# Kernel tuning notes

Hardware: AMD Instinct MI355X
Metric: run time of the kernel (lower is better)

## Reference

```python
import jax, jax.numpy as jnp
import numpy as np

B, L, DM, H, PD = 2, 1024, 512, 8, 64
D = DM // H  # head_dim = 64
NEG = -10000.0


def setup_inputs() -> dict:
    key = jax.random.key(0)
    ks = jax.random.split(key, 12)
    s = 1.0 / np.sqrt(DM)
    sp = 1.0 / np.sqrt(PD)
    return {
        "x": jax.random.normal(ks[0], (B, L, DM), dtype=jnp.float32),
        "z": jax.random.normal(ks[1], (B, L, L, PD), dtype=jnp.float32),
        "residue_mask": jnp.ones((B, L), dtype=bool),
        "Wq": jax.random.normal(ks[2], (DM, DM), dtype=jnp.float32) * s,
        "bq": jnp.zeros((DM,), dtype=jnp.float32),
        "Wk": jax.random.normal(ks[3], (DM, DM), dtype=jnp.float32) * s,
        "bk": jnp.zeros((DM,), dtype=jnp.float32),
        "Wv": jax.random.normal(ks[4], (DM, DM), dtype=jnp.float32) * s,
        "bv": jnp.zeros((DM,), dtype=jnp.float32),
        "Wo": jax.random.normal(ks[5], (DM, DM), dtype=jnp.float32) * s,
        "bo": jnp.zeros((DM,), dtype=jnp.float32),
        "Wpb": jax.random.normal(ks[6], (PD, H), dtype=jnp.float32) * sp,
    }


def reference(x, z, residue_mask, Wq, bq, Wk, bk, Wv, bv, Wo, bo, Wpb):
    b, l, c = x.shape
    scale = 1.0 / np.sqrt(D)
    # projections -> (B, H, L, D)
    q = (x @ Wq + bq).reshape(b, l, H, D).transpose(0, 2, 1, 3)
    k = (x @ Wk + bk).reshape(b, l, H, D).transpose(0, 2, 1, 3)
    v = (x @ Wv + bv).reshape(b, l, H, D).transpose(0, 2, 1, 3)
    # pair bias: (B, L, L, PD) @ (PD, H) -> (B, H, L, L)
    bias = jnp.einsum('bijp,ph->bhij', z, Wpb)
    logits = jnp.einsum('bhid,bhjd->bhij', q, k) * scale + bias
    key_ok = residue_mask[:, None, None, :]
    query_ok = residue_mask[:, None, :, None]
    logits = jnp.where(key_ok, logits, NEG)
    logits = jnp.where(query_ok, logits, NEG)
    attn = jax.nn.softmax(logits, axis=-1)
    out = jnp.einsum('bhij,bhjd->bhid', attn, v)
    out = out.transpose(0, 2, 1, 3).reshape(b, l, c)
    return out @ Wo + bo
```

## Files before the change

### kernel.cpp

```cpp
#include <hip/hip_runtime.h>

typedef __bf16 bf16;
typedef __attribute__((ext_vector_type(4))) __bf16 bf16x4;
typedef __attribute__((ext_vector_type(8))) __bf16 bf16x8;
typedef __attribute__((ext_vector_type(4))) float f32x4;
typedef __attribute__((ext_vector_type(4))) _Float16 f16x4;
typedef __attribute__((ext_vector_type(2))) _Float16 f16x2;

#define B_   2
#define L_   1024
#define DM_  512
#define H_   8
#define D_   64
#define PD_  64
#define NEG_VAL -10000.0f

#define WTPB_N (16*64)

static __device__ __forceinline__ f32x4 mfma_bf16(bf16x8 a, bf16x8 b, f32x4 c) {
  return __builtin_amdgcn_mfma_f32_16x16x32_bf16(a, b, c, 0, 0, 0);
}

__global__ __launch_bounds__(256) void prep_kernel(
    const float* __restrict__ x, const float* __restrict__ Wq, const float* __restrict__ Wk,
    const float* __restrict__ Wv, const float* __restrict__ Wo, const float* __restrict__ Wpb,
    bf16* __restrict__ xb, bf16* __restrict__ Wt, bf16* __restrict__ Wto, bf16* __restrict__ Wtpb) {
  __shared__ float td[32][33];
  int bid = blockIdx.x, tid = threadIdx.x;
  if (bid < 1024) {
    int r = tid >> 3, c4 = (tid & 7) * 4;
    const float* src;
    bf16* dstbase;
    int n0, k0, srcol;
    if (bid < 768) {
      int nt2 = bid >> 4, kt = bid & 15;
      n0 = nt2 * 32; k0 = kt * 32;
      int sel = n0 >> 9;
      src = sel == 0 ? Wq : (sel == 1 ? Wk : Wv);
      srcol = n0 & 511;
      dstbase = Wt + (long)n0 * 512;
    } else {
      int t2 = bid - 768;
      int nt2 = t2 >> 4, kt = t2 & 15;
      n0 = nt2 * 32; k0 = kt * 32;
      src = Wo; srcol = n0;
      dstbase = Wto + (long)n0 * 512;
    }
    f32x4 v = *reinterpret_cast<const f32x4*>(src + (long)(k0 + r) * 512 + srcol + c4);
#pragma unroll
    for (int e = 0; e < 4; ++e) td[r][c4 + e] = v[e];
    __syncthreads();
    int nl = tid >> 3, k4 = (tid & 7) * 4;
    bf16x4 o;
#pragma unroll
    for (int e = 0; e < 4; ++e) o[e] = (bf16)td[k4 + e][nl];
    *reinterpret_cast<bf16x4*>(dstbase + (long)nl * 512 + k0 + k4) = o;
  } else if (bid < 2048) {
    int base = (bid - 1024) * 1024 + tid * 4;
    f32x4 v = *reinterpret_cast<const f32x4*>(x + base);
    bf16x4 o;
#pragma unroll
    for (int e = 0; e < 4; ++e) o[e] = (bf16)v[e];
    *reinterpret_cast<bf16x4*>(xb + base) = o;
  } else {
    for (int t = tid; t < WTPB_N; t += 256) {
      int n = t >> 6, kk = t & 63;
      Wtpb[t] = (n < 8) ? (bf16)Wpb[kk * 8 + n] : (bf16)0.0f;
    }
  }
}

__global__ __launch_bounds__(256) void qkv_gemm(
    const bf16* __restrict__ xb, const bf16* __restrict__ Wt,
    const float* __restrict__ bq, const float* __restrict__ bk, const float* __restrict__ bv,
    bf16* __restrict__ qb, bf16* __restrict__ kb, bf16* __restrict__ vT) {
  int wid = blockIdx.x * 4 + (threadIdx.x >> 6);
  int lane = threadIdx.x & 63;
  int mt = wid / 48, nt = wid - mt * 48;
  int row0 = mt * 32, col0 = nt * 32;
  int lr = lane & 15, lg = lane >> 4;
  const bf16* a0p = xb + (row0 + lr) * 512 + lg * 8;
  const bf16* a1p = a0p + 16 * 512;
  const bf16* b0p = Wt + (col0 + lr) * 512 + lg * 8;
  const bf16* b1p = b0p + 16 * 512;
  f32x4 acc00 = {0.f,0.f,0.f,0.f}, acc01 = acc00, acc10 = acc00, acc11 = acc00;
#pragma unroll
  for (int kk = 0; kk < 512; kk += 32) {
    bf16x8 a0 = *reinterpret_cast<const bf16x8*>(a0p + kk);
    bf16x8 a1 = *reinterpret_cast<const bf16x8*>(a1p + kk);
    bf16x8 b0 = *reinterpret_cast<const bf16x8*>(b0p + kk);
    bf16x8 b1 = *reinterpret_cast<const bf16x8*>(b1p + kk);
    acc00 = mfma_bf16(a0, b0, acc00);
    acc01 = mfma_bf16(a0, b1, acc01);
    acc10 = mfma_bf16(a1, b0, acc10);
    acc11 = mfma_bf16(a1, b1, acc11);
  }
#pragma unroll
  for (int ni = 0; ni < 2; ++ni) {
    int col = col0 + ni * 16 + lr;
    int wsel = col >> 9;
    int ncol = col & 511;
    int h = ncol >> 6, d = ncol & 63;
    const float* bias = wsel == 0 ? bq : (wsel == 1 ? bk : bv);
    float bval = bias[ncol];
#pragma unroll
    for (int mi = 0; mi < 2; ++mi) {
      f32x4 acc = (mi == 0) ? (ni == 0 ? acc00 : acc01) : (ni == 0 ? acc10 : acc11);
      int m0 = row0 + mi * 16 + lg * 4;
      int bidx = m0 >> 10, l0 = m0 & 1023;
      if (wsel == 2) {
        bf16x4 pv;
#pragma unroll
        for (int r = 0; r < 4; ++r) pv[r] = (bf16)(acc[r] + bval);
        *reinterpret_cast<bf16x4*>(vT + ((long)(bidx * H_ + h) * D_ + d) * L_ + l0) = pv;
      } else if (wsel == 0) {
#pragma unroll
        for (int r = 0; r < 4; ++r)
          qb[((long)(bidx * H_ + h) * L_ + l0 + r) * D_ + d] = (bf16)((acc[r] + bval) * 0.125f);
      } else {
#pragma unroll
        for (int r = 0; r < 4; ++r)
          kb[((long)(bidx * H_ + h) * L_ + l0 + r) * D_ + d] = (bf16)(acc[r] + bval);
      }
    }
  }
}

__global__ __launch_bounds__(256) void bias_gemm(
    const float* __restrict__ z, const bf16* __restrict__ Wtpb, const int* __restrict__ mask,
    _Float16* __restrict__ biasbuf) {
  __shared__ _Float16 outt[8][1032];
  int tid = threadIdx.x, w = tid >> 6, lane = tid & 63;
  int lr = lane & 15, lg = lane >> 4;
  int bid = blockIdx.x;
  int jc = bid & 15, it = (bid >> 4) & 63, b = bid >> 10;
  bf16x8 wb0 = *reinterpret_cast<const bf16x8*>(Wtpb + lr * 64 + lg * 8);
  bf16x8 wb1 = *reinterpret_cast<const bf16x8*>(Wtpb + lr * 64 + 32 + lg * 8);
#pragma unroll
  for (int ii = 0; ii < 4; ++ii) {
    int il = w * 4 + ii;
    int i = it * 16 + il;
#pragma unroll
    for (int js = 0; js < 4; ++js) {
      const float* zr = z + ((long)(b * L_ + i) * L_ + jc * 64 + js * 16 + lr) * 64 + lg * 8;
      f32x4 z0 = *reinterpret_cast<const f32x4*>(zr);
      f32x4 z1 = *reinterpret_cast<const f32x4*>(zr + 4);
      f32x4 z2 = *reinterpret_cast<const f32x4*>(zr + 32);
      f32x4 z3 = *reinterpret_cast<const f32x4*>(zr + 36);
      bf16x8 a0, a1;
#pragma unroll
      for (int e = 0; e < 4; ++e) {
        a0[e] = (bf16)z0[e]; a0[e + 4] = (bf16)z1[e];
        a1[e] = (bf16)z2[e]; a1[e + 4] = (bf16)z3[e];
      }
      f32x4 c = {0.f, 0.f, 0.f, 0.f};
      c = mfma_bf16(a0, wb0, c);
      c = mfma_bf16(a1, wb1, c);
      if (lr < 8) {
        int4 mk = *reinterpret_cast<const int4*>(mask + b * L_ + jc * 64 + js * 16 + lg * 4);
        f16x4 hv;
        hv[0] = mk.x ? (_Float16)c[0] : (_Float16)NEG_VAL;
        hv[1] = mk.y ? (_Float16)c[1] : (_Float16)NEG_VAL;
        hv[2] = mk.z ? (_Float16)c[2] : (_Float16)NEG_VAL;
        hv[3] = mk.w ? (_Float16)c[3] : (_Float16)NEG_VAL;
        *reinterpret_cast<f16x4*>(&outt[lr][((js * 4 + lg) * 16 + il) * 4]) = hv;
      }
    }
  }
  __syncthreads();
  {
    int h = tid & 7, part = tid >> 3;
    _Float16* dst = biasbuf + (((((long)b * H_ + h) * 64 + it) * 16 + jc) << 10) + part * 32;
    const _Float16* srcl = &outt[h][part * 32];
#pragma unroll
    for (int e = 0; e < 8; ++e)
      *reinterpret_cast<f16x4*>(dst + e * 4) = *reinterpret_cast<const f16x4*>(srcl + e * 4);
  }
}

__global__ __launch_bounds__(256) void attn_kernel(
    const bf16* __restrict__ qb, const bf16* __restrict__ kb, const bf16* __restrict__ vT,
    const _Float16* __restrict__ biasb, const int* __restrict__ mask, bf16* __restrict__ attn_out) {
  __shared__ bf16 p_lds[4][16 * 64];
  __shared__ float o_lds[4][16][64];
  __shared__ float m_lds[4][16];
  __shared__ float l_lds[4][16];
  int bid = blockIdx.x;
  int b = bid >> 9, h = (bid >> 6) & 7, it = bid & 63;
  int i0 = it * 16;
  int tid = threadIdx.x, w = tid >> 6, lane = tid & 63, lr = lane & 15, lg = lane >> 4;

  const bf16* qrow = qb + ((long)(b * H_ + h) * L_ + i0 + lr) * D_ + lg * 8;
  bf16x8 qa0 = *reinterpret_cast<const bf16x8*>(qrow);
  bf16x8 qa1 = *reinterpret_cast<const bf16x8*>(qrow + 32);
  const bf16* kbase = kb + (long)(b * H_ + h) * L_ * D_;
  const bf16* vbase = vT + (long)(b * H_ + h) * D_ * L_;
  const _Float16* bias_base = biasb + ((((long)(b * H_ + h) * 64 + it)) << 14);
  bool qok = mask[b * L_ + i0 + lr] != 0;

  float m = -3.0e38f, l = 0.f;
  f32x4 o0 = {0.f,0.f,0.f,0.f}, o1 = o0, o2 = o0, o3 = o0;
  char* pbuf = (char*)&p_lds[w][0];
  int swz = (lr & 7) << 4;

  for (int jt = 0; jt < 4; ++jt) {
    int j0 = w * 256 + jt * 64;
    const _Float16* btile = bias_base + ((w * 4 + jt) << 10);
    f32x4 s0, s1, s2, s3;
#pragma unroll
    for (int tile = 0; tile < 4; ++tile) {
      f16x4 bv = *reinterpret_cast<const f16x4*>(btile + ((tile * 4 + lg) * 16 + lr) * 4);
      f32x4 acc;
#pragma unroll
      for (int r = 0; r < 4; ++r) acc[r] = (float)bv[r];
      const bf16* kr = kbase + (long)(j0 + tile * 16 + lr) * D_ + lg * 8;
      acc = mfma_bf16(*reinterpret_cast<const bf16x8*>(kr), qa0, acc);
      acc = mfma_bf16(*reinterpret_cast<const bf16x8*>(kr + 32), qa1, acc);
      if (tile == 0) s0 = acc; else if (tile == 1) s1 = acc; else if (tile == 2) s2 = acc; else s3 = acc;
    }
    if (!qok) {
#pragma unroll
      for (int r = 0; r < 4; ++r) { s0[r] = NEG_VAL; s1[r] = NEG_VAL; s2[r] = NEG_VAL; s3[r] = NEG_VAL; }
    }
    float mt = s0[0];
#pragma unroll
    for (int r = 0; r < 4; ++r) mt = fmaxf(fmaxf(fmaxf(mt, s0[r]), fmaxf(s1[r], s2[r])), s3[r]);
    mt = fmaxf(mt, __shfl_xor(mt, 16));
    mt = fmaxf(mt, __shfl_xor(mt, 32));
    float mnew = fmaxf(m, mt);
    float alpha = __expf(m - mnew);
    m = mnew;
    f32x4 p0, p1, p2, p3;
    float ps = 0.f;
#pragma unroll
    for (int r = 0; r < 4; ++r) {
      p0[r] = __expf(s0[r] - mnew); p1[r] = __expf(s1[r] - mnew);
      p2[r] = __expf(s2[r] - mnew); p3[r] = __expf(s3[r] - mnew);
      ps += p0[r] + p1[r] + p2[r] + p3[r];
    }
    ps += __shfl_xor(ps, 16);
    ps += __shfl_xor(ps, 32);
    l = l * alpha + ps;
#pragma unroll
    for (int r = 0; r < 4; ++r) { o0[r] *= alpha; o1[r] *= alpha; o2[r] *= alpha; o3[r] *= alpha; }
#pragma unroll
    for (int tile = 0; tile < 4; ++tile) {
      f32x4 pv = (tile == 0) ? p0 : (tile == 1) ? p1 : (tile == 2) ? p2 : p3;
      bf16x4 pb_;
#pragma unroll
      for (int r = 0; r < 4; ++r) pb_[r] = (bf16)pv[r];
      *reinterpret_cast<bf16x4*>(pbuf + ((lr * 128 + tile * 32 + lg * 8) ^ swz)) = pb_;
    }
    bf16x8 pa0 = *reinterpret_cast<const bf16x8*>(pbuf + ((lr * 128 + lg * 16) ^ swz));
    bf16x8 pa1 = *reinterpret_cast<const bf16x8*>(pbuf + ((lr * 128 + 64 + lg * 16) ^ swz));
#pragma unroll
    for (int dtile = 0; dtile < 4; ++dtile) {
      const bf16* vr = vbase + (long)(dtile * 16 + lr) * L_ + j0 + lg * 8;
      f32x4 acc = (dtile == 0) ? o0 : (dtile == 1) ? o1 : (dtile == 2) ? o2 : o3;
      acc = mfma_bf16(*reinterpret_cast<const bf16x8*>(vr), pa0, acc);
      acc = mfma_bf16(*reinterpret_cast<const bf16x8*>(vr + 32), pa1, acc);
      if (dtile == 0) o0 = acc; else if (dtile == 1) o1 = acc; else if (dtile == 2) o2 = acc; else o3 = acc;
    }
  }
#pragma unroll
  for (int dtile = 0; dtile < 4; ++dtile) {
    f32x4 ov = (dtile == 0) ? o0 : (dtile == 1) ? o1 : (dtile == 2) ? o2 : o3;
    *reinterpret_cast<f32x4*>(&o_lds[w][lr][dtile * 16 + lg * 4]) = ov;
  }
  if (lg == 0) { m_lds[w][lr] = m; l_lds[w][lr] = l; }
  __syncthreads();
  {
    int row = tid >> 4, d0 = (tid & 15) * 4;
    float M = fmaxf(fmaxf(m_lds[0][row], m_lds[1][row]), fmaxf(m_lds[2][row], m_lds[3][row]));
    float lt = 0.f;
    float oacc[4] = {0.f, 0.f, 0.f, 0.f};
#pragma unroll
    for (int ww = 0; ww < 4; ++ww) {
      float c = __expf(m_lds[ww][row] - M);
      lt += c * l_lds[ww][row];
#pragma unroll
      for (int e = 0; e < 4; ++e) oacc[e] += c * o_lds[ww][row][d0 + e];
    }
    float inv = 1.0f / lt;
    bf16x4 ov;
#pragma unroll
    for (int e = 0; e < 4; ++e) ov[e] = (bf16)(oacc[e] * inv);
    *reinterpret_cast<bf16x4*>(attn_out + ((long)(b * L_ + i0 + row)) * DM_ + h * D_ + d0) = ov;
  }
}

__global__ __launch_bounds__(256) void out_gemm(
    const bf16* __restrict__ ab, const bf16* __restrict__ Wto,
    const float* __restrict__ bo, float* __restrict__ out) {
  int wid = blockIdx.x * 4 + (threadIdx.x >> 6);
  int lane = threadIdx.x & 63;
  int mt = wid >> 4, nt = wid & 15;
  int row0 = mt * 32, col0 = nt * 32;
  int lr = lane & 15, lg = lane >> 4;
  const bf16* a0p = ab + (row0 + lr) * 512 + lg * 8;
  const bf16* a1p = a0p + 16 * 512;
  const bf16* b0p = Wto + (col0 + lr) * 512 + lg * 8;
  const bf16* b1p = b0p + 16 * 512;
  f32x4 acc00 = {0.f,0.f,0.f,0.f}, acc01 = acc00, acc10 = acc00, acc11 = acc00;
#pragma unroll
  for (int kk = 0; kk < 512; kk += 32) {
    bf16x8 a0 = *reinterpret_cast<const bf16x8*>(a0p + kk);
    bf16x8 a1 = *reinterpret_cast<const bf16x8*>(a1p + kk);
    bf16x8 b0 = *reinterpret_cast<const bf16x8*>(b0p + kk);
    bf16x8 b1 = *reinterpret_cast<const bf16x8*>(b1p + kk);
    acc00 = mfma_bf16(a0, b0, acc00);
    acc01 = mfma_bf16(a0, b1, acc01);
    acc10 = mfma_bf16(a1, b0, acc10);
    acc11 = mfma_bf16(a1, b1, acc11);
  }
#pragma unroll
  for (int ni = 0; ni < 2; ++ni) {
    int col = col0 + ni * 16 + lr;
    float bval = bo[col];
#pragma unroll
    for (int mi = 0; mi < 2; ++mi) {
      f32x4 acc = (mi == 0) ? (ni == 0 ? acc00 : acc01) : (ni == 0 ? acc10 : acc11);
      int m0 = row0 + mi * 16 + lg * 4;
#pragma unroll
      for (int r = 0; r < 4; ++r) out[(long)(m0 + r) * 512 + col] = acc[r] + bval;
    }
  }
}

extern "C" void kernel_launch(void* const* d_in, const int* in_sizes, int n_in,
                              void* d_out, int out_size, void* d_ws, size_t ws_size,
                              hipStream_t stream) {
  const float* x    = (const float*)d_in[0];
  const float* z    = (const float*)d_in[1];
  const int*   mask = (const int*)d_in[2];
  const float* Wq   = (const float*)d_in[3];
  const float* bq   = (const float*)d_in[4];
  const float* Wk   = (const float*)d_in[5];
  const float* bk   = (const float*)d_in[6];
  const float* Wv   = (const float*)d_in[7];
  const float* bv   = (const float*)d_in[8];
  const float* Wo   = (const float*)d_in[9];
  const float* bo   = (const float*)d_in[10];
  const float* Wpb  = (const float*)d_in[11];

  char* ws = (char*)d_ws;
  bf16* xb        = (bf16*)(ws + 0);
  bf16* Wt        = (bf16*)(ws + 2097152);
  bf16* Wto       = (bf16*)(ws + 3670016);
  bf16* Wtpb      = (bf16*)(ws + 4194304);
  bf16* qbuf      = (bf16*)(ws + 4196352);
  bf16* kbuf      = (bf16*)(ws + 6293504);
  bf16* vTbuf     = (bf16*)(ws + 8390656);
  bf16* attn_out  = (bf16*)(ws + 10487808);
  _Float16* biasb = (_Float16*)(ws + 12584960);

  prep_kernel<<<2049, 256, 0, stream>>>(x, Wq, Wk, Wv, Wo, Wpb, xb, Wt, Wto, Wtpb);
  qkv_gemm<<<768, 256, 0, stream>>>(xb, Wt, bq, bk, bv, qbuf, kbuf, vTbuf);
  bias_gemm<<<2048, 256, 0, stream>>>(z, Wtpb, mask, biasb);
  attn_kernel<<<1024, 256, 0, stream>>>(qbuf, kbuf, vTbuf, biasb, mask, attn_out);
  out_gemm<<<256, 256, 0, stream>>>(attn_out, Wto, bo, (float*)d_out);
}
```

Measured before the change: 193.7 us.

## Fuse pair-bias GEMM into prep kernel and stage QKV weight panel in LDS

The pair-bias projection over z now runs in the same launch as the weight/x conversion blocks, with Wpb staged in shared memory and converted per block. This removes one kernel launch and lets the bias work overlap the conversion work. The QKV GEMM is retiled so each block shares a 16-column weight panel held in LDS across four waves, which cuts redundant global weight loads. The attention output staging buffer is padded to reduce LDS bank conflicts. The trade-off is a larger LDS footprint for the fused kernel and more QKV blocks, each doing less work.

```diff
diff --git a/kernel.cpp b/kernel.cpp
--- a/kernel.cpp
+++ b/kernel.cpp
@@ -15,57 +15,113 @@
 #define PD_  64
 #define NEG_VAL -10000.0f
 
-#define WTPB_N (16*64)
-
 static __device__ __forceinline__ f32x4 mfma_bf16(bf16x8 a, bf16x8 b, f32x4 c) {
   return __builtin_amdgcn_mfma_f32_16x16x32_bf16(a, b, c, 0, 0, 0);
 }
 
-__global__ __launch_bounds__(256) void prep_kernel(
+__global__ __launch_bounds__(256) void prep_bias(
+    const float* __restrict__ z, const float* __restrict__ Wpb, const int* __restrict__ mask,
     const float* __restrict__ x, const float* __restrict__ Wq, const float* __restrict__ Wk,
-    const float* __restrict__ Wv, const float* __restrict__ Wo, const float* __restrict__ Wpb,
-    bf16* __restrict__ xb, bf16* __restrict__ Wt, bf16* __restrict__ Wto, bf16* __restrict__ Wtpb) {
-  __shared__ float td[32][33];
+    const float* __restrict__ Wv, const float* __restrict__ Wo,
+    _Float16* __restrict__ biasbuf, bf16* __restrict__ xb, bf16* __restrict__ Wt,
+    bf16* __restrict__ Wto) {
+  __shared__ char smem[18944];
   int bid = blockIdx.x, tid = threadIdx.x;
-  if (bid < 1024) {
-    int r = tid >> 3, c4 = (tid & 7) * 4;
-    const float* src;
-    bf16* dstbase;
-    int n0, k0, srcol;
-    if (bid < 768) {
-      int nt2 = bid >> 4, kt = bid & 15;
-      n0 = nt2 * 32; k0 = kt * 32;
-      int sel = n0 >> 9;
-      src = sel == 0 ? Wq : (sel == 1 ? Wk : Wv);
-      srcol = n0 & 511;
-      dstbase = Wt + (long)n0 * 512;
+  if (bid < 2048) {
+    _Float16 (*outt)[1032] = (_Float16(*)[1032])smem;
+    float* wpb_lds = (float*)(smem + 16512);
+    int w = tid >> 6, lane = tid & 63;
+    int lr = lane & 15, lg = lane >> 4;
+    int jc = bid & 15, it = (bid >> 4) & 63, b = bid >> 10;
+    if (tid < 128) {
+      f32x4 v = reinterpret_cast<const f32x4*>(Wpb)[tid];
+      *reinterpret_cast<f32x4*>(wpb_lds + tid * 4) = v;
+    }
+    __syncthreads();
+    bf16x8 wb0, wb1;
+#pragma unroll
+    for (int e = 0; e < 8; ++e) {
+      wb0[e] = (lr < 8) ? (bf16)wpb_lds[(lg * 8 + e) * 8 + lr] : (bf16)0.0f;
+      wb1[e] = (lr < 8) ? (bf16)wpb_lds[(lg * 8 + 32 + e) * 8 + lr] : (bf16)0.0f;
+    }
+#pragma unroll
+    for (int ii = 0; ii < 4; ++ii) {
+      int il = w * 4 + ii;
+      int i = it * 16 + il;
+#pragma unroll
+      for (int js = 0; js < 4; ++js) {
+        const float* zr = z + ((long)(b * L_ + i) * L_ + jc * 64 + js * 16 + lr) * 64 + lg * 8;
+        f32x4 z0 = *reinterpret_cast<const f32x4*>(zr);
+        f32x4 z1 = *reinterpret_cast<const f32x4*>(zr + 4);
+        f32x4 z2 = *reinterpret_cast<const f32x4*>(zr + 32);
+        f32x4 z3 = *reinterpret_cast<const f32x4*>(zr + 36);
+        bf16x8 a0, a1;
+#pragma unroll
+        for (int e = 0; e < 4; ++e) {
+          a0[e] = (bf16)z0[e]; a0[e + 4] = (bf16)z1[e];
+          a1[e] = (bf16)z2[e]; a1[e + 4] = (bf16)z3[e];
+        }
+        f32x4 c = {0.f, 0.f, 0.f, 0.f};
+        c = mfma_bf16(a0, wb0, c);
+        c = mfma_bf16(a1, wb1, c);
+        if (lr < 8) {
+          int4 mk = *reinterpret_cast<const int4*>(mask + b * L_ + jc * 64 + js * 16 + lg * 4);
+          f16x4 hv;
+          hv[0] = mk.x ? (_Float16)c[0] : (_Float16)NEG_VAL;
+          hv[1] = mk.y ? (_Float16)c[1] : (_Float16)NEG_VAL;
+          hv[2] = mk.z ? (_Float16)c[2] : (_Float16)NEG_VAL;
+          hv[3] = mk.w ? (_Float16)c[3] : (_Float16)NEG_VAL;
+          *reinterpret_cast<f16x4*>(&outt[lr][((js * 4 + lg) * 16 + il) * 4]) = hv;
+        }
+      }
+    }
+    __syncthreads();
+    {
+      int h = tid & 7, part = tid >> 3;
+      _Float16* dst = biasbuf + (((((long)b * H_ + h) * 64 + it) * 16 + jc) << 10) + part * 32;
+      const _Float16* srcl = &outt[h][part * 32];
+#pragma unroll
+      for (int e = 0; e < 8; ++e)
+        *reinterpret_cast<f16x4*>(dst + e * 4) = *reinterpret_cast<const f16x4*>(srcl + e * 4);
+    }
+  } else {
+    int pbid = bid - 2048;
+    if (pbid < 1024) {
+      float (*td)[33] = (float(*)[33])smem;
+      int r = tid >> 3, c4 = (tid & 7) * 4;
+      const float* src;
+      bf16* dstbase;
+      int n0, k0, srcol;
+      if (pbid < 768) {
+        int nt2 = pbid >> 4, kt = pbid & 15;
+        n0 = nt2 * 32; k0 = kt * 32;
+        int sel = n0 >> 9;
+        src = sel == 0 ? Wq : (sel == 1 ? Wk : Wv);
+        srcol = n0 & 511;
+        dstbase = Wt + (long)n0 * 512;
+      } else {
+        int t2 = pbid - 768;
+        int nt2 = t2 >> 4, kt = t2 & 15;
+        n0 = nt2 * 32; k0 = kt * 32;
+        src = Wo; srcol = n0;
+        dstbase = Wto + (long)n0 * 512;
+      }
+      f32x4 v = *reinterpret_cast<const f32x4*>(src + (long)(k0 + r) * 512 + srcol + c4);
+#pragma unroll
+      for (int e = 0; e < 4; ++e) td[r][c4 + e] = v[e];
+      __syncthreads();
+      int nl = tid >> 3, k4 = (tid & 7) * 4;
+      bf16x4 o;
+#pragma unroll
+      for (int e = 0; e < 4; ++e) o[e] = (bf16)td[k4 + e][nl];
+      *reinterpret_cast<bf16x4*>(dstbase + (long)nl * 512 + k0 + k4) = o;
     } else {
-      int t2 = bid - 768;
-      int nt2 = t2 >> 4, kt = t2 & 15;
-      n0 = nt2 * 32; k0 = kt * 32;
-      src = Wo; srcol = n0;
-      dstbase = Wto + (long)n0 * 512;
-    }
-    f32x4 v = *reinterpret_cast<const f32x4*>(src + (long)(k0 + r) * 512 + srcol + c4);
-#pragma unroll
-    for (int e = 0; e < 4; ++e) td[r][c4 + e] = v[e];
-    __syncthreads();
-    int nl = tid >> 3, k4 = (tid & 7) * 4;
-    bf16x4 o;
-#pragma unroll
-    for (int e = 0; e < 4; ++e) o[e] = (bf16)td[k4 + e][nl];
-    *reinterpret_cast<bf16x4*>(dstbase + (long)nl * 512 + k0 + k4) = o;
-  } else if (bid < 2048) {
-    int base = (bid - 1024) * 1024 + tid * 4;
-    f32x4 v = *reinterpret_cast<const f32x4*>(x + base);
-    bf16x4 o;
-#pragma unroll
-    for (int e = 0; e < 4; ++e) o[e] = (bf16)v[e];
-    *reinterpret_cast<bf16x4*>(xb + base) = o;
-  } else {
-    for (int t = tid; t < WTPB_N; t += 256) {
-      int n = t >> 6, kk = t & 63;
-      Wtpb[t] = (n < 8) ? (bf16)Wpb[kk * 8 + n] : (bf16)0.0f;
+      int base = (pbid - 1024) * 1024 + tid * 4;
+      f32x4 v = *reinterpret_cast<const f32x4*>(x + base);
+      bf16x4 o;
+#pragma unroll
+      for (int e = 0; e < 4; ++e) o[e] = (bf16)v[e];
+      *reinterpret_cast<bf16x4*>(xb + base) = o;
     }
   }
 }
@@ -74,107 +130,60 @@
     const bf16* __restrict__ xb, const bf16* __restrict__ Wt,
     const float* __restrict__ bq, const float* __restrict__ bk, const float* __restrict__ bv,
     bf16* __restrict__ qb, bf16* __restrict__ kb, bf16* __restrict__ vT) {
-  int wid = blockIdx.x * 4 + (threadIdx.x >> 6);
-  int lane = threadIdx.x & 63;
-  int mt = wid / 48, nt = wid - mt * 48;
-  int row0 = mt * 32, col0 = nt * 32;
+  __shared__ bf16 bpanel[16 * 520];
+  int tid = threadIdx.x, w = tid >> 6, lane = tid & 63;
   int lr = lane & 15, lg = lane >> 4;
-  const bf16* a0p = xb + (row0 + lr) * 512 + lg * 8;
+  int bid = blockIdx.x;
+  int mt = bid / 96, nt = bid - mt * 96;
+  int col0 = nt * 16;
+  {
+    const bf16* src = Wt + (long)col0 * 512;
+#pragma unroll
+    for (int q = 0; q < 4; ++q) {
+      int off = q * 2048 + tid * 8;
+      int row = off >> 9, col = off & 511;
+      *reinterpret_cast<bf16x8*>(&bpanel[row * 520 + col]) =
+          *reinterpret_cast<const bf16x8*>(src + off);
+    }
+  }
+  __syncthreads();
+  int m0base = mt * 128 + w * 32;
+  const bf16* a0p = xb + (long)(m0base + lr) * 512 + lg * 8;
   const bf16* a1p = a0p + 16 * 512;
-  const bf16* b0p = Wt + (col0 + lr) * 512 + lg * 8;
-  const bf16* b1p = b0p + 16 * 512;
-  f32x4 acc00 = {0.f,0.f,0.f,0.f}, acc01 = acc00, acc10 = acc00, acc11 = acc00;
+  f32x4 acc0 = {0.f, 0.f, 0.f, 0.f}, acc1 = acc0;
 #pragma unroll
   for (int kk = 0; kk < 512; kk += 32) {
     bf16x8 a0 = *reinterpret_cast<const bf16x8*>(a0p + kk);
     bf16x8 a1 = *reinterpret_cast<const bf16x8*>(a1p + kk);
-    bf16x8 b0 = *reinterpret_cast<const bf16x8*>(b0p + kk);
-    bf16x8 b1 = *reinterpret_cast<const bf16x8*>(b1p + kk);
-    acc00 = mfma_bf16(a0, b0, acc00);
-    acc01 = mfma_bf16(a0, b1, acc01);
-    acc10 = mfma_bf16(a1, b0, acc10);
-    acc11 = mfma_bf16(a1, b1, acc11);
-  }
-#pragma unroll
-  for (int ni = 0; ni < 2; ++ni) {
-    int col = col0 + ni * 16 + lr;
-    int wsel = col >> 9;
-    int ncol = col & 511;
-    int h = ncol >> 6, d = ncol & 63;
-    const float* bias = wsel == 0 ? bq : (wsel == 1 ? bk : bv);
-    float bval = bias[ncol];
-#pragma unroll
-    for (int mi = 0; mi < 2; ++mi) {
-      f32x4 acc = (mi == 0) ? (ni == 0 ? acc00 : acc01) : (ni == 0 ? acc10 : acc11);
-      int m0 = row0 + mi * 16 + lg * 4;
-      int bidx = m0 >> 10, l0 = m0 & 1023;
-      if (wsel == 2) {
-        bf16x4 pv;
-#pragma unroll
-        for (int r = 0; r < 4; ++r) pv[r] = (bf16)(acc[r] + bval);
-        *reinterpret_cast<bf16x4*>(vT + ((long)(bidx * H_ + h) * D_ + d) * L_ + l0) = pv;
-      } else if (wsel == 0) {
-#pragma unroll
-        for (int r = 0; r < 4; ++r)
-          qb[((long)(bidx * H_ + h) * L_ + l0 + r) * D_ + d] = (bf16)((acc[r] + bval) * 0.125f);
-      } else {
-#pragma unroll
-        for (int r = 0; r < 4; ++r)
-          kb[((long)(bidx * H_ + h) * L_ + l0 + r) * D_ + d] = (bf16)(acc[r] + bval);
-      }
-    }
-  }
-}
-
-__global__ __launch_bounds__(256) void bias_gemm(
-    const float* __restrict__ z, const bf16* __restrict__ Wtpb, const int* __restrict__ mask,
-    _Float16* __restrict__ biasbuf) {
-  __shared__ _Float16 outt[8][1032];
-  int tid = threadIdx.x, w = tid >> 6, lane = tid & 63;
-  int lr = lane & 15, lg = lane >> 4;
-  int bid = blockIdx.x;
-  int jc = bid & 15, it = (bid >> 4) & 63, b = bid >> 10;
-  bf16x8 wb0 = *reinterpret_cast<const bf16x8*>(Wtpb + lr * 64 + lg * 8);
-  bf16x8 wb1 = *reinterpret_cast<const bf16x8*>(Wtpb + lr * 64 + 32 + lg * 8);
-#pragma unroll
-  for (int ii = 0; ii < 4; ++ii) {
-    int il = w * 4 + ii;
-    int i = it * 16 + il;
-#pragma unroll
-    for (int js = 0; js < 4; ++js) {
-      const float* zr = z + ((long)(b * L_ + i) * L_ + jc * 64 + js * 16 + lr) * 64 + lg * 8;
-      f32x4 z0 = *reinterpret_cast<const f32x4*>(zr);
-      f32x4 z1 = *reinterpret_cast<const f32x4*>(zr + 4);
-      f32x4 z2 = *reinterpret_cast<const f32x4*>(zr + 32);
-      f32x4 z3 = *reinterpret_cast<const f32x4*>(zr + 36);
-      bf16x8 a0, a1;
-#pragma unroll
-      for (int e = 0; e < 4; ++e) {
-        a0[e] = (bf16)z0[e]; a0[e + 4] = (bf16)z1[e];
-        a1[e] = (bf16)z2[e]; a1[e + 4] = (bf16)z3[e];
-      }
-      f32x4 c = {0.f, 0.f, 0.f, 0.f};
-      c = mfma_bf16(a0, wb0, c);
-      c = mfma_bf16(a1, wb1, c);
-      if (lr < 8) {
-        int4 mk = *reinterpret_cast<const int4*>(mask + b * L_ + jc * 64 + js * 16 + lg * 4);
-        f16x4 hv;
-        hv[0] = mk.x ? (_Float16)c[0] : (_Float16)NEG_VAL;
-        hv[1] = mk.y ? (_Float16)c[1] : (_Float16)NEG_VAL;
-        hv[2] = mk.z ? (_Float16)c[2] : (_Float16)NEG_VAL;
-        hv[3] = mk.w ? (_Float16)c[3] : (_Float16)NEG_VAL;
-        *reinterpret_cast<f16x4*>(&outt[lr][((js * 4 + lg) * 16 + il) * 4]) = hv;
-      }
-    }
-  }
-  __syncthreads();
-  {
-    int h = tid & 7, part = tid >> 3;
-    _Float16* dst = biasbuf + (((((long)b * H_ + h) * 64 + it) * 16 + jc) << 10) + part * 32;
-    const _Float16* srcl = &outt[h][part * 32];
-#pragma unroll
-    for (int e = 0; e < 8; ++e)
-      *reinterpret_cast<f16x4*>(dst + e * 4) = *reinterpret_cast<const f16x4*>(srcl + e * 4);
+    bf16x8 b = *reinterpret_cast<const bf16x8*>(&bpanel[lr * 520 + kk + lg * 8]);
+    acc0 = mfma_bf16(a0, b, acc0);
+    acc1 = mfma_bf16(a1, b, acc1);
+  }
+  int col = col0 + lr;
+  int wsel = col >> 9;
+  int ncol = col & 511;
+  int h = ncol >> 6, d = ncol & 63;
+  const float* bias = wsel == 0 ? bq : (wsel == 1 ? bk : bv);
+  float bval = bias[ncol];
+#pragma unroll
+  for (int mi = 0; mi < 2; ++mi) {
+    f32x4 acc = (mi == 0) ? acc0 : acc1;
+    int m0 = m0base + mi * 16 + lg * 4;
+    int bidx = m0 >> 10, l0 = m0 & 1023;
+    if (wsel == 2) {
+      bf16x4 pv;
+#pragma unroll
+      for (int r = 0; r < 4; ++r) pv[r] = (bf16)(acc[r] + bval);
+      *reinterpret_cast<bf16x4*>(vT + ((long)(bidx * H_ + h) * D_ + d) * L_ + l0) = pv;
+    } else if (wsel == 0) {
+#pragma unroll
+      for (int r = 0; r < 4; ++r)
+        qb[((long)(bidx * H_ + h) * L_ + l0 + r) * D_ + d] = (bf16)((acc[r] + bval) * 0.125f);
+    } else {
+#pragma unroll
+      for (int r = 0; r < 4; ++r)
+        kb[((long)(bidx * H_ + h) * L_ + l0 + r) * D_ + d] = (bf16)(acc[r] + bval);
+    }
   }
 }
 
@@ -182,7 +191,7 @@
     const bf16* __restrict__ qb, const bf16* __restrict__ kb, const bf16* __restrict__ vT,
     const _Float16* __restrict__ biasb, const int* __restrict__ mask, bf16* __restrict__ attn_out) {
   __shared__ bf16 p_lds[4][16 * 64];
-  __shared__ float o_lds[4][16][64];
+  __shared__ float o_lds[4][16][68];
   __shared__ float m_lds[4][16];
   __shared__ float l_lds[4][16];
   int bid = blockIdx.x;
@@ -347,16 +356,15 @@
   bf16* xb        = (bf16*)(ws + 0);
   bf16* Wt        = (bf16*)(ws + 2097152);
   bf16* Wto       = (bf16*)(ws + 3670016);
-  bf16* Wtpb      = (bf16*)(ws + 4194304);
   bf16* qbuf      = (bf16*)(ws + 4196352);
   bf16* kbuf      = (bf16*)(ws + 6293504);
   bf16* vTbuf     = (bf16*)(ws + 8390656);
   bf16* attn_out  = (bf16*)(ws + 10487808);
   _Float16* biasb = (_Float16*)(ws + 12584960);
 
-  prep_kernel<<<2049, 256, 0, stream>>>(x, Wq, Wk, Wv, Wo, Wpb, xb, Wt, Wto, Wtpb);
-  qkv_gemm<<<768, 256, 0, stream>>>(xb, Wt, bq, bk, bv, qbuf, kbuf, vTbuf);
-  bias_gemm<<<2048, 256, 0, stream>>>(z, Wtpb, mask, biasb);
+  prep_bias<<<4096, 256, 0, stream>>>(z, Wpb, mask, x, Wq, Wk, Wv, Wo,
+                                      biasb, xb, Wt, Wto);
+  qkv_gemm<<<1536, 256, 0, stream>>>(xb, Wt, bq, bk, bv, qbuf, kbuf, vTbuf);
   attn_kernel<<<1024, 256, 0, stream>>>(qbuf, kbuf, vTbuf, biasb, mask, attn_out);
   out_gemm<<<256, 256, 0, stream>>>(attn_out, Wto, bo, (float*)d_out);
 }
```

New measurement: 186.4 us. 1.04x faster.
